# Kernel optimization log

Hardware: AMD Instinct MI355X
Metric: run time of the kernel (lower is better)

## Reference

```python
import jax, jax.numpy as jnp
import numpy as np

HID = 64
PRE = 14


def _lstm_last(x, Wih, Whh, b):
    # x: (B, T, F) batch_first; single-layer torch LSTM; returns last hidden (B, H)
    H = Whh.shape[1]
    def step(carry, xt):
        h, c = carry
        g = xt @ Wih.T + h @ Whh.T + b  # gates order i,f,g,o (torch convention)
        i, f, gg, o = jnp.split(g, 4, axis=-1)
        c = jax.nn.sigmoid(f) * c + jax.nn.sigmoid(i) * jnp.tanh(gg)
        h = jax.nn.sigmoid(o) * jnp.tanh(c)
        return (h, c), None
    h0 = jnp.zeros((x.shape[0], H), x.dtype)
    (h, _), _ = jax.lax.scan(step, (h0, h0), jnp.swapaxes(x, 0, 1))
    return h


def _sircell(beta, gamma, c, sir):
    # beta,gamma: (B,N,1); c: (B,N,N); sir: (B,N,3); beta_incorporated=False branch
    eps = 1e-8
    S, I, R = sir[..., 0:1], sir[..., 1:2], sir[..., 2:3]
    Ntot = jnp.maximum(S + I + R, eps)
    infection = c @ I                      # (B,N,1) graph diffusion of infected
    dS = -beta * S / Ntot * infection
    dI = -dS - gamma * I
    dR = gamma * I
    S_t = jnp.maximum(S + dS, 0.0)
    I_t = jnp.maximum(I + dI, 0.0)
    R_t = jnp.maximum(R + dR, 0.0)
    scale = Ntot / jnp.maximum(S_t + I_t + R_t, eps)
    I_new = jnp.maximum(-dS, 0.0)
    return jnp.concatenate([I_new, S_t * scale, I_t * scale, R_t * scale], axis=-1)


def reference(x_s, x, bWih, bWhh, bb, bfW, bfb, gWih, gWhh, gb, gfW, gfb, cWih, cWhh, cb, cfW, cfb):
    B, T, N, F = x_s.shape
    P = bfW.shape[0]
    xs = jnp.transpose(x_s, (0, 2, 1, 3)).reshape(B * N, T, F)
    betas = jax.nn.sigmoid(_lstm_last(xs, bWih, bWhh, bb) @ bfW.T + bfb).reshape(B, N, P, 1)
    gammas = jax.nn.sigmoid(_lstm_last(xs, gWih, gWhh, gb) @ gfW.T + gfb).reshape(B, N, P, 1)
    xst = jnp.transpose(x_s, (0, 2, 1, 3))                       # (B,N,T,F)
    Hi = jnp.broadcast_to(xst[:, :, None], (B, N, N, T, F))
    Hj = jnp.broadcast_to(xst[:, None], (B, N, N, T, F))
    edge = jnp.concatenate([Hi, Hj], -1).reshape(B * N * N, T, 2 * F)
    cij = jax.nn.sigmoid(_lstm_last(edge, cWih, cWhh, cb) @ cfW.T + cfb).reshape(B, N, N, P)
    cij = jax.nn.softmax(jnp.transpose(cij, (0, 3, 1, 2)), axis=-1)  # (B,P,N,N)
    cs = jnp.transpose(cij, (0, 2, 1, 3))                            # (B,N,P,N)

    def step(sir, inp):
        bt, gt, ct = inp
        nsir = _sircell(bt, gt, ct, sir)
        return nsir[:, :, 1:], nsir

    _, outs = jax.lax.scan(
        step, x[:, -1],
        (jnp.transpose(betas, (2, 0, 1, 3)),
         jnp.transpose(gammas, (2, 0, 1, 3)),
         jnp.transpose(cs, (2, 0, 1, 3))))
    out = jnp.transpose(outs, (1, 0, 2, 3))                          # (B,P,N,4)
    epi = jnp.transpose(jnp.concatenate([betas, gammas, cs], -1), (0, 2, 1, 3))  # (B,P,N,N+2)
    return out[..., 2:3], epi, out[..., 1:], out[..., 0:1]


def setup_inputs() -> dict:
    key = jax.random.key(0)
    ks = jax.random.split(key, 20)
    B, T, N, F = 4, 12, 128, 3
    H, P = HID, PRE
    s = 1.0 / np.sqrt(H)
    def u(k, shape):
        return jax.random.uniform(k, shape, jnp.float32, -s, s)
    inp = {
        'x_s': jax.random.normal(ks[0], (B, T, N, F), jnp.float32),
        'x': jax.random.uniform(ks[1], (B, T, N, F), jnp.float32),
        'bWih': u(ks[2], (4 * H, F)), 'bWhh': u(ks[3], (4 * H, H)), 'bb': u(ks[4], (4 * H,)),
        'bfW': u(ks[5], (P, H)), 'bfb': u(ks[6], (P,)),
        'gWih': u(ks[7], (4 * H, F)), 'gWhh': u(ks[8], (4 * H, H)), 'gb': u(ks[9], (4 * H,)),
        'gfW': u(ks[10], (P, H)), 'gfb': u(ks[11], (P,)),
        'cWih': u(ks[12], (4 * H, 2 * F)), 'cWhh': u(ks[13], (4 * H, H)), 'cb': u(ks[14], (4 * H,)),
        'cfW': u(ks[15], (P, H)), 'cfb': u(ks[16], (P,)),
    }
    return inp
```

## Files before the change

kernel.cpp:

```cpp
#include <hip/hip_runtime.h>

#define TT 12
#define NN 128
#define BB 4
#define PP 14

typedef __attribute__((ext_vector_type(8))) short short8;
typedef __attribute__((ext_vector_type(4))) float f32x4;
typedef __attribute__((ext_vector_type(2))) float float2v;
typedef __attribute__((ext_vector_type(2))) unsigned uint2v;

__device__ inline unsigned short f2bf(float x){
  unsigned u = __builtin_bit_cast(unsigned, x);
  u += 0x7fffu + ((u >> 16) & 1u);
  return (unsigned short)(u >> 16);
}
__device__ inline float bf2f(unsigned short h){
  unsigned u = ((unsigned)h) << 16;
  return __builtin_bit_cast(float, u);
}
__device__ inline float fexp2(float x){ return __builtin_amdgcn_exp2f(x); }
__device__ inline float sigf(float x){ return __builtin_amdgcn_rcpf(1.0f + fexp2(x * -1.44269504f)); }

__device__ inline float2v exp2v(float2v x){
  float2v r; r[0]=__builtin_amdgcn_exp2f(x[0]); r[1]=__builtin_amdgcn_exp2f(x[1]); return r;
}
__device__ inline float2v rcpv(float2v x){
  float2v r; r[0]=__builtin_amdgcn_rcpf(x[0]); r[1]=__builtin_amdgcn_rcpf(x[1]); return r;
}
__device__ inline float2v sigp(float2v xp){ return rcpv(1.0f + exp2v(xp)); }
__device__ inline float2v tanhp(float2v xp){ return 1.0f - 2.0f*rcpv(1.0f + exp2v(xp)); }

__global__ __launch_bounds__(256) void lstm_all(
    const float* __restrict__ x_s,
    const float* __restrict__ bWih, const float* __restrict__ bWhh, const float* __restrict__ bb_,
    const float* __restrict__ bfW,  const float* __restrict__ bfb,
    const float* __restrict__ gWih, const float* __restrict__ gWhh, const float* __restrict__ gb_,
    const float* __restrict__ gfW,  const float* __restrict__ gfb,
    const float* __restrict__ cWih, const float* __restrict__ cWhh, const float* __restrict__ cb_,
    const float* __restrict__ cfW,  const float* __restrict__ cfb,
    float* __restrict__ out_epi,
    float* __restrict__ betas_ws, float* __restrict__ gammas_ws)
{
  __shared__ __align__(16) char hbuf[2*4096];
  __shared__ __align__(16) unsigned short xext[TT*32*8];
  __shared__ float fw_lds[PP*64];
  __shared__ float fb_lds[PP];

  const int tid = threadIdx.x;
  const int l = tid & 63, w = tid >> 6;
  const int col = l & 15, q = l >> 4;

  const int rot = (col & 7) << 4;
  const int r0offA = col*128 + ((  0 + (q<<4) + rot) & 127);
  const int r1offA = col*128 + (( 64 + (q<<4) + rot) & 127);
  const int wroffA = col*128 + ((w*32 + q*8 + rot) & 127);
  const int r0offB = r0offA + 2048;
  const int r1offB = r1offA + 2048;
  const int wroffB = wroffA + 2048;

  int g0 = blockIdx.x << 1;
  int mode; const float *Wih, *Whh, *bias, *fW, *fb;
  if (g0 < 4096)      { mode=0; Wih=cWih; Whh=cWhh; bias=cb_; fW=cfW; fb=cfb; }
  else if (g0 < 4128) { mode=1; g0-=4096; Wih=bWih; Whh=bWhh; bias=bb_; fW=bfW; fb=bfb; }
  else                { mode=2; g0-=4128; Wih=gWih; Whh=gWhh; bias=gb_; fW=gfW; fb=gfb; }

  int b, i=0, s0;
  if (mode==0) { b = g0 >> 10; int rem = g0 & 1023; i = rem >> 3; s0 = (rem & 7) << 4; }
  else         { b = g0 >> 3; s0 = (g0 & 7) << 4; }

  for (int task = tid; task < TT*32; task += 256) {
    int t = task >> 5, m = task & 31;
    unsigned short* dst = &xext[(t*32+m)*8];
    float v0=0,v1=0,v2=0,v3=0,v4=0,v5=0,v6=0,v7=0;
    if (mode==0) {
      const float* xi = x_s + ((b*TT + t)*NN + i)*3;
      const float* xj = x_s + ((b*TT + t)*NN + (s0+m))*3;
      v0=xi[0]; v1=xi[1]; v2=xi[2]; v3=xj[0]; v4=xj[1]; v5=xj[2]; v6=1.f;
    } else {
      const float* xn = x_s + ((b*TT + t)*NN + (s0+m))*3;
      v0=xn[0]; v1=xn[1]; v2=xn[2]; v3=1.f;
    }
    dst[0]=f2bf(v0); dst[1]=f2bf(v1); dst[2]=f2bf(v2); dst[3]=f2bf(v3);
    dst[4]=f2bf(v4); dst[5]=f2bf(v5); dst[6]=f2bf(v6); dst[7]=f2bf(v7);
  }
  for (int idx = tid; idx < 1024; idx += 256) ((unsigned*)hbuf)[idx] = 0;
  for (int idx = tid; idx < PP*64; idx += 256) fw_lds[idx] = fW[idx];
  if (tid < PP) fb_lds[tid] = fb[tid];

  short8 Aw[4][2]; short8 Ax[4];
  #pragma unroll
  for (int gt = 0; gt < 4; ++gt) {
    float sc = (gt==2) ? 2.88539008f : -1.44269504f;
    int gate = gt*64 + w*16 + col;
    #pragma unroll
    for (int kt = 0; kt < 2; ++kt) {
      const float* src = Whh + gate*64 + kt*32 + q*8;
      short8 fr;
      #pragma unroll
      for (int jj = 0; jj < 8; ++jj) fr[jj] = (short)f2bf(src[jj]*sc);
      Aw[gt][kt] = fr;
    }
    short8 ax = {0,0,0,0,0,0,0,0};
    if (q == 0) {
      if (mode==0) {
        ax[0]=(short)f2bf(Wih[gate*6+0]*sc); ax[1]=(short)f2bf(Wih[gate*6+1]*sc); ax[2]=(short)f2bf(Wih[gate*6+2]*sc);
        ax[3]=(short)f2bf(Wih[gate*6+3]*sc); ax[4]=(short)f2bf(Wih[gate*6+4]*sc); ax[5]=(short)f2bf(Wih[gate*6+5]*sc);
        ax[6]=(short)f2bf(bias[gate]*sc);
      } else {
        ax[0]=(short)f2bf(Wih[gate*3+0]*sc); ax[1]=(short)f2bf(Wih[gate*3+1]*sc); ax[2]=(short)f2bf(Wih[gate*3+2]*sc);
        ax[3]=(short)f2bf(bias[gate]*sc);
      }
    }
    Ax[gt] = ax;
  }

  __syncthreads();

  float2v cA0 = {0.f,0.f}, cA1 = {0.f,0.f}, cB0 = {0.f,0.f}, cB1 = {0.f,0.f};
  const short8 zero8 = {0,0,0,0,0,0,0,0};

#define MM(acc, aop, bop) acc = __builtin_amdgcn_mfma_f32_16x16x32_bf16(aop, bop, acc, 0,0,0)

  for (int t = 0; t < TT; ++t) {
    const char* rb = hbuf + ((t & 1) ? 4096 : 0);
    char* wbp      = hbuf + ((t & 1) ? 0 : 4096);
    short8 b0a = *(const short8*)(rb + r0offA);
    short8 b1a = *(const short8*)(rb + r1offA);
    short8 b0b = *(const short8*)(rb + r0offB);
    short8 b1b = *(const short8*)(rb + r1offB);
    short8 bxa = zero8, bxb = zero8;
    if (l < 16) {
      bxa = *(const short8*)&xext[(t*32 + col)*8];
      bxb = *(const short8*)&xext[(t*32 + 16 + col)*8];
    }
    f32x4 Fa = {0.f,0.f,0.f,0.f}, Ia = Fa, Ga = Fa, Oa = Fa;
    f32x4 Fb = Fa, Ib = Fa, Gb = Fa, Ob = Fa;
    MM(Fa, Aw[1][0], b0a); MM(Fb, Aw[1][0], b0b);
    MM(Ia, Aw[0][0], b0a); MM(Ib, Aw[0][0], b0b);
    MM(Ga, Aw[2][0], b0a); MM(Gb, Aw[2][0], b0b);
    MM(Oa, Aw[3][0], b0a); MM(Ob, Aw[3][0], b0b);
    MM(Fa, Aw[1][1], b1a); MM(Fb, Aw[1][1], b1b);
    MM(Ia, Aw[0][1], b1a); MM(Ib, Aw[0][1], b1b);
    MM(Ga, Aw[2][1], b1a); MM(Gb, Aw[2][1], b1b);
    MM(Oa, Aw[3][1], b1a); MM(Ob, Aw[3][1], b1b);
    MM(Fa, Ax[1], bxa);    MM(Fb, Ax[1], bxb);
    MM(Ia, Ax[0], bxa);    MM(Ib, Ax[0], bxb);
    MM(Ga, Ax[2], bxa);    MM(Gb, Ax[2], bxb);
    MM(Oa, Ax[3], bxa);    MM(Ob, Ax[3], bxb);

    {
      float2v f0 = {Fa[0],Fa[1]}, f1 = {Fa[2],Fa[3]};
      float2v i0 = {Ia[0],Ia[1]}, i1 = {Ia[2],Ia[3]};
      float2v g0v = {Ga[0],Ga[1]}, g1v = {Ga[2],Ga[3]};
      float2v o0 = {Oa[0],Oa[1]}, o1 = {Oa[2],Oa[3]};
      cA0 = sigp(f0)*cA0 + sigp(i0)*tanhp(g0v);
      cA1 = sigp(f1)*cA1 + sigp(i1)*tanhp(g1v);
      float2v tc0 = 1.0f - 2.0f*rcpv(1.0f + exp2v(cA0 * 2.88539008f));
      float2v tc1 = 1.0f - 2.0f*rcpv(1.0f + exp2v(cA1 * 2.88539008f));
      float2v h0 = sigp(o0)*tc0;
      float2v h1 = sigp(o1)*tc1;
      unsigned plo, phi;
      asm("v_cvt_pk_bf16_f32 %0, %1, %2" : "=v"(plo) : "v"(h0[0]), "v"(h0[1]));
      asm("v_cvt_pk_bf16_f32 %0, %1, %2" : "=v"(phi) : "v"(h1[0]), "v"(h1[1]));
      uint2v pv = {plo, phi};
      *(uint2v*)(wbp + wroffA) = pv;
    }
    {
      float2v f0 = {Fb[0],Fb[1]}, f1 = {Fb[2],Fb[3]};
      float2v i0 = {Ib[0],Ib[1]}, i1 = {Ib[2],Ib[3]};
      float2v g0v = {Gb[0],Gb[1]}, g1v = {Gb[2],Gb[3]};
      float2v o0 = {Ob[0],Ob[1]}, o1 = {Ob[2],Ob[3]};
      cB0 = sigp(f0)*cB0 + sigp(i0)*tanhp(g0v);
      cB1 = sigp(f1)*cB1 + sigp(i1)*tanhp(g1v);
      float2v tc0 = 1.0f - 2.0f*rcpv(1.0f + exp2v(cB0 * 2.88539008f));
      float2v tc1 = 1.0f - 2.0f*rcpv(1.0f + exp2v(cB1 * 2.88539008f));
      float2v h0 = sigp(o0)*tc0;
      float2v h1 = sigp(o1)*tc1;
      unsigned plo, phi;
      asm("v_cvt_pk_bf16_f32 %0, %1, %2" : "=v"(plo) : "v"(h0[0]), "v"(h0[1]));
      asm("v_cvt_pk_bf16_f32 %0, %1, %2" : "=v"(phi) : "v"(h1[0]), "v"(h1[1]));
      uint2v pv = {plo, phi};
      *(uint2v*)(wbp + wroffB) = pv;
    }
    __syncthreads();
  }
#undef MM

  const char* hfin = hbuf;
  for (int task = tid; task < 32*PP; task += 256) {
    int seq = task & 31, p = task >> 5;
    int rot2 = (seq & 7) << 4;
    float dot = fb_lds[p];
    #pragma unroll
    for (int kc = 0; kc < 8; ++kc) {
      short8 v = *(const short8*)(hfin + seq*128 + (((kc<<4) + rot2) & 127));
      #pragma unroll
      for (int jj = 0; jj < 8; ++jj)
        dot += bf2f((unsigned short)v[jj]) * fw_lds[p*64 + kc*8 + jj];
    }
    float val = sigf(dot);
    if (mode==0) {
      out_epi[(size_t)((b*PP + p)*NN + i)*130 + 2 + (s0+seq)] = val;
    } else if (mode==1) {
      betas_ws[(b*NN + s0+seq)*PP + p] = val;
    } else {
      gammas_ws[(b*NN + s0+seq)*PP + p] = val;
    }
  }
}

__global__ __launch_bounds__(256) void softmax_epi(
    const float* __restrict__ betas_ws, const float* __restrict__ gammas_ws,
    float* __restrict__ out_epi)
{
  int row = blockIdx.x*4 + (threadIdx.x >> 6);
  int l = threadIdx.x & 63;
  int b = row / (PP*NN); int rem = row - b*(PP*NN); int p = rem >> 7; int i = rem & 127;
  float* epi = out_epi + (size_t)row*130;
  float v0 = epi[2+l], v1 = epi[2+64+l];
  float m = fmaxf(v0, v1);
  #pragma unroll
  for (int off = 32; off; off >>= 1) m = fmaxf(m, __shfl_xor(m, off));
  float e0 = fexp2((v0-m)*1.44269504f), e1 = fexp2((v1-m)*1.44269504f);
  float s = e0 + e1;
  #pragma unroll
  for (int off = 32; off; off >>= 1) s += __shfl_xor(s, off);
  float inv = 1.0f / s;
  epi[2+l] = e0*inv; epi[2+64+l] = e1*inv;
  if (l == 0) epi[0] = betas_ws[(b*NN+i)*PP + p];
  if (l == 1) epi[1] = gammas_ws[(b*NN+i)*PP + p];
}

__global__ __launch_bounds__(1024) void sir_scan(
    const float* __restrict__ x,
    const float* __restrict__ betas_ws, const float* __restrict__ gammas_ws,
    const float* __restrict__ epi,
    float* __restrict__ out0, float* __restrict__ out2, float* __restrict__ out3)
{
  __shared__ float Ish[NN];
  int b = blockIdx.x;
  int tid = threadIdx.x;
  int i = tid >> 3, q = tid & 7;
  const float* x0 = x + ((b*TT + 11)*NN + i)*3;
  float S = x0[0], I = x0[1], R = x0[2];
  if (q == 0) Ish[i] = I;

  float2v v[8], vn[8];
  {
    const float* crow = epi + (size_t)((b*PP + 0)*NN + i)*130 + 2 + q*16;
    #pragma unroll
    for (int jj = 0; jj < 8; ++jj) v[jj] = *(const float2v*)(crow + jj*2);
  }
  __syncthreads();
  for (int p = 0; p < PP; ++p) {
    if (p+1 < PP) {
      const float* crow = epi + (size_t)((b*PP + p+1)*NN + i)*130 + 2 + q*16;
      #pragma unroll
      for (int jj = 0; jj < 8; ++jj) vn[jj] = *(const float2v*)(crow + jj*2);
    }
    float part = 0.f;
    #pragma unroll
    for (int jj = 0; jj < 8; ++jj)
      part += v[jj][0]*Ish[q*16 + jj*2] + v[jj][1]*Ish[q*16 + jj*2 + 1];
    part += __shfl_xor(part, 1);
    part += __shfl_xor(part, 2);
    part += __shfl_xor(part, 4);
    __syncthreads();
    if (q == 0) {
      float beta  = betas_ws[(b*NN+i)*PP + p];
      float gamma = gammas_ws[(b*NN+i)*PP + p];
      float Ntot = fmaxf(S+I+R, 1e-8f);
      float dS = -beta*S/Ntot*part;
      float dI = -dS - gamma*I;
      float dR = gamma*I;
      float St = fmaxf(S+dS, 0.f), It = fmaxf(I+dI, 0.f), Rt = fmaxf(R+dR, 0.f);
      float scale = Ntot / fmaxf(St+It+Rt, 1e-8f);
      float Inew = fmaxf(-dS, 0.f);
      int o = (b*PP+p)*NN + i;
      float Sn = St*scale, In = It*scale, Rn = Rt*scale;
      out0[o] = In;
      out2[o*3+0] = Sn; out2[o*3+1] = In; out2[o*3+2] = Rn;
      out3[o] = Inew;
      S = Sn; I = In; R = Rn;
      Ish[i] = I;
    }
    #pragma unroll
    for (int jj = 0; jj < 8; ++jj) v[jj] = vn[jj];
    __syncthreads();
  }
}

extern "C" void kernel_launch(void* const* d_in, const int* in_sizes, int n_in,
                              void* d_out, int out_size, void* d_ws, size_t ws_size,
                              hipStream_t stream) {
  const float* x_s  = (const float*)d_in[0];
  const float* x    = (const float*)d_in[1];
  const float* bWih = (const float*)d_in[2];
  const float* bWhh = (const float*)d_in[3];
  const float* bb_  = (const float*)d_in[4];
  const float* bfW  = (const float*)d_in[5];
  const float* bfb  = (const float*)d_in[6];
  const float* gWih = (const float*)d_in[7];
  const float* gWhh = (const float*)d_in[8];
  const float* gb_  = (const float*)d_in[9];
  const float* gfW  = (const float*)d_in[10];
  const float* gfb  = (const float*)d_in[11];
  const float* cWih = (const float*)d_in[12];
  const float* cWhh = (const float*)d_in[13];
  const float* cb_  = (const float*)d_in[14];
  const float* cfW  = (const float*)d_in[15];
  const float* cfb  = (const float*)d_in[16];

  float* out  = (float*)d_out;
  float* out0 = out;
  float* epi  = out + 7168;
  float* out2 = out + 7168 + 931840;
  float* out3 = out + 7168 + 931840 + 21504;
  float* betas_ws  = (float*)d_ws;
  float* gammas_ws = betas_ws + 7168;

  hipLaunchKernelGGL(lstm_all, dim3(2080), dim3(256), 0, stream,
      x_s, bWih,bWhh,bb_,bfW,bfb, gWih,gWhh,gb_,gfW,gfb, cWih,cWhh,cb_,cfW,cfb,
      epi, betas_ws, gammas_ws);
  hipLaunchKernelGGL(softmax_epi, dim3(1792), dim3(256), 0, stream,
      betas_ws, gammas_ws, epi);
  hipLaunchKernelGGL(sir_scan, dim3(4), dim3(1024), 0, stream,
      x, betas_ws, gammas_ws, epi, out0, out2, out3);
}
```

Before: 113.3 us.

## Fuse softmax into SIR scan, merge LSTM cell transcendentals, drop lane guard

```diff
diff --git a/kernel.cpp b/kernel.cpp
--- a/kernel.cpp
+++ b/kernel.cpp
@@ -20,7 +20,8 @@
   return __builtin_bit_cast(float, u);
 }
 __device__ inline float fexp2(float x){ return __builtin_amdgcn_exp2f(x); }
-__device__ inline float sigf(float x){ return __builtin_amdgcn_rcpf(1.0f + fexp2(x * -1.44269504f)); }
+__device__ inline float frcp(float x){ return __builtin_amdgcn_rcpf(x); }
+__device__ inline float sigf(float x){ return frcp(1.0f + fexp2(x * -1.44269504f)); }
 
 __device__ inline float2v exp2v(float2v x){
   float2v r; r[0]=__builtin_amdgcn_exp2f(x[0]); r[1]=__builtin_amdgcn_exp2f(x[1]); return r;
@@ -28,8 +29,6 @@
 __device__ inline float2v rcpv(float2v x){
   float2v r; r[0]=__builtin_amdgcn_rcpf(x[0]); r[1]=__builtin_amdgcn_rcpf(x[1]); return r;
 }
-__device__ inline float2v sigp(float2v xp){ return rcpv(1.0f + exp2v(xp)); }
-__device__ inline float2v tanhp(float2v xp){ return 1.0f - 2.0f*rcpv(1.0f + exp2v(xp)); }
 
 __global__ __launch_bounds__(256) void lstm_all(
     const float* __restrict__ x_s,
@@ -118,9 +117,16 @@
   __syncthreads();
 
   float2v cA0 = {0.f,0.f}, cA1 = {0.f,0.f}, cB0 = {0.f,0.f}, cB1 = {0.f,0.f};
-  const short8 zero8 = {0,0,0,0,0,0,0,0};
 
 #define MM(acc, aop, bop) acc = __builtin_amdgcn_mfma_f32_16x16x32_bf16(aop, bop, acc, 0,0,0)
+#define CELL(cvar, hvar, fF, fI, fG, fO) { \
+    float2v Ei = exp2v(fI), Ef = exp2v(fF), Eg = exp2v(fG), Eo = exp2v(fO); \
+    float2v t1 = (Ei + 1.0f) * (Eg + 1.0f); \
+    float2v pf = Ef + 1.0f; \
+    float2v num = cvar * t1 + pf * (Eg - 1.0f); \
+    cvar = num * rcpv(pf * t1); \
+    float2v Ec = exp2v(cvar * 2.88539008f); \
+    hvar = (Ec - 1.0f) * rcpv((Ec + 1.0f) * (Eo + 1.0f)); }
 
   for (int t = 0; t < TT; ++t) {
     const char* rb = hbuf + ((t & 1) ? 4096 : 0);
@@ -129,11 +135,8 @@
     short8 b1a = *(const short8*)(rb + r1offA);
     short8 b0b = *(const short8*)(rb + r0offB);
     short8 b1b = *(const short8*)(rb + r1offB);
-    short8 bxa = zero8, bxb = zero8;
-    if (l < 16) {
-      bxa = *(const short8*)&xext[(t*32 + col)*8];
-      bxb = *(const short8*)&xext[(t*32 + 16 + col)*8];
-    }
+    short8 bxa = *(const short8*)&xext[(t*32 + col)*8];
+    short8 bxb = *(const short8*)&xext[(t*32 + 16 + col)*8];
     f32x4 Fa = {0.f,0.f,0.f,0.f}, Ia = Fa, Ga = Fa, Oa = Fa;
     f32x4 Fb = Fa, Ib = Fa, Gb = Fa, Ob = Fa;
     MM(Fa, Aw[1][0], b0a); MM(Fb, Aw[1][0], b0b);
@@ -154,12 +157,9 @@
       float2v i0 = {Ia[0],Ia[1]}, i1 = {Ia[2],Ia[3]};
       float2v g0v = {Ga[0],Ga[1]}, g1v = {Ga[2],Ga[3]};
       float2v o0 = {Oa[0],Oa[1]}, o1 = {Oa[2],Oa[3]};
-      cA0 = sigp(f0)*cA0 + sigp(i0)*tanhp(g0v);
-      cA1 = sigp(f1)*cA1 + sigp(i1)*tanhp(g1v);
-      float2v tc0 = 1.0f - 2.0f*rcpv(1.0f + exp2v(cA0 * 2.88539008f));
-      float2v tc1 = 1.0f - 2.0f*rcpv(1.0f + exp2v(cA1 * 2.88539008f));
-      float2v h0 = sigp(o0)*tc0;
-      float2v h1 = sigp(o1)*tc1;
+      float2v h0, h1;
+      CELL(cA0, h0, f0, i0, g0v, o0);
+      CELL(cA1, h1, f1, i1, g1v, o1);
       unsigned plo, phi;
       asm("v_cvt_pk_bf16_f32 %0, %1, %2" : "=v"(plo) : "v"(h0[0]), "v"(h0[1]));
       asm("v_cvt_pk_bf16_f32 %0, %1, %2" : "=v"(phi) : "v"(h1[0]), "v"(h1[1]));
@@ -171,12 +171,9 @@
       float2v i0 = {Ib[0],Ib[1]}, i1 = {Ib[2],Ib[3]};
       float2v g0v = {Gb[0],Gb[1]}, g1v = {Gb[2],Gb[3]};
       float2v o0 = {Ob[0],Ob[1]}, o1 = {Ob[2],Ob[3]};
-      cB0 = sigp(f0)*cB0 + sigp(i0)*tanhp(g0v);
-      cB1 = sigp(f1)*cB1 + sigp(i1)*tanhp(g1v);
-      float2v tc0 = 1.0f - 2.0f*rcpv(1.0f + exp2v(cB0 * 2.88539008f));
-      float2v tc1 = 1.0f - 2.0f*rcpv(1.0f + exp2v(cB1 * 2.88539008f));
-      float2v h0 = sigp(o0)*tc0;
-      float2v h1 = sigp(o1)*tc1;
+      float2v h0, h1;
+      CELL(cB0, h0, f0, i0, g0v, o0);
+      CELL(cB1, h1, f1, i1, g1v, o1);
       unsigned plo, phi;
       asm("v_cvt_pk_bf16_f32 %0, %1, %2" : "=v"(plo) : "v"(h0[0]), "v"(h0[1]));
       asm("v_cvt_pk_bf16_f32 %0, %1, %2" : "=v"(phi) : "v"(h1[0]), "v"(h1[1]));
@@ -186,6 +183,7 @@
     __syncthreads();
   }
 #undef MM
+#undef CELL
 
   const char* hfin = hbuf;
   for (int task = tid; task < 32*PP; task += 256) {
@@ -204,38 +202,18 @@
       out_epi[(size_t)((b*PP + p)*NN + i)*130 + 2 + (s0+seq)] = val;
     } else if (mode==1) {
       betas_ws[(b*NN + s0+seq)*PP + p] = val;
+      out_epi[(size_t)((b*PP + p)*NN + (s0+seq))*130 + 0] = val;
     } else {
       gammas_ws[(b*NN + s0+seq)*PP + p] = val;
-    }
-  }
-}
-
-__global__ __launch_bounds__(256) void softmax_epi(
-    const float* __restrict__ betas_ws, const float* __restrict__ gammas_ws,
-    float* __restrict__ out_epi)
-{
-  int row = blockIdx.x*4 + (threadIdx.x >> 6);
-  int l = threadIdx.x & 63;
-  int b = row / (PP*NN); int rem = row - b*(PP*NN); int p = rem >> 7; int i = rem & 127;
-  float* epi = out_epi + (size_t)row*130;
-  float v0 = epi[2+l], v1 = epi[2+64+l];
-  float m = fmaxf(v0, v1);
-  #pragma unroll
-  for (int off = 32; off; off >>= 1) m = fmaxf(m, __shfl_xor(m, off));
-  float e0 = fexp2((v0-m)*1.44269504f), e1 = fexp2((v1-m)*1.44269504f);
-  float s = e0 + e1;
-  #pragma unroll
-  for (int off = 32; off; off >>= 1) s += __shfl_xor(s, off);
-  float inv = 1.0f / s;
-  epi[2+l] = e0*inv; epi[2+64+l] = e1*inv;
-  if (l == 0) epi[0] = betas_ws[(b*NN+i)*PP + p];
-  if (l == 1) epi[1] = gammas_ws[(b*NN+i)*PP + p];
+      out_epi[(size_t)((b*PP + p)*NN + (s0+seq))*130 + 1] = val;
+    }
+  }
 }
 
 __global__ __launch_bounds__(1024) void sir_scan(
     const float* __restrict__ x,
     const float* __restrict__ betas_ws, const float* __restrict__ gammas_ws,
-    const float* __restrict__ epi,
+    float* __restrict__ epi,
     float* __restrict__ out0, float* __restrict__ out2, float* __restrict__ out3)
 {
   __shared__ float Ish[NN];
@@ -259,13 +237,33 @@
       #pragma unroll
       for (int jj = 0; jj < 8; ++jj) vn[jj] = *(const float2v*)(crow + jj*2);
     }
+    float2v e[8];
+    float s = 0.f;
+    #pragma unroll
+    for (int jj = 0; jj < 8; ++jj) {
+      float2v ev; ev[0] = fexp2(v[jj][0]*1.44269504f); ev[1] = fexp2(v[jj][1]*1.44269504f);
+      e[jj] = ev; s += ev[0] + ev[1];
+    }
+    s += __shfl_xor(s, 1);
+    s += __shfl_xor(s, 2);
+    s += __shfl_xor(s, 4);
+    float inv = frcp(s);
     float part = 0.f;
     #pragma unroll
     for (int jj = 0; jj < 8; ++jj)
-      part += v[jj][0]*Ish[q*16 + jj*2] + v[jj][1]*Ish[q*16 + jj*2 + 1];
+      part += e[jj][0]*Ish[q*16 + jj*2] + e[jj][1]*Ish[q*16 + jj*2 + 1];
     part += __shfl_xor(part, 1);
     part += __shfl_xor(part, 2);
     part += __shfl_xor(part, 4);
+    part *= inv;
+    {
+      float* crow = epi + (size_t)((b*PP + p)*NN + i)*130 + 2 + q*16;
+      #pragma unroll
+      for (int jj = 0; jj < 8; ++jj) {
+        float2v nv = {e[jj][0]*inv, e[jj][1]*inv};
+        *(float2v*)(crow + jj*2) = nv;
+      }
+    }
     __syncthreads();
     if (q == 0) {
       float beta  = betas_ws[(b*NN+i)*PP + p];
@@ -323,8 +321,6 @@
   hipLaunchKernelGGL(lstm_all, dim3(2080), dim3(256), 0, stream,
       x_s, bWih,bWhh,bb_,bfW,bfb, gWih,gWhh,gb_,gfW,gfb, cWih,cWhh,cb_,cfW,cfb,
       epi, betas_ws, gammas_ws);
-  hipLaunchKernelGGL(softmax_epi, dim3(1792), dim3(256), 0, stream,
-      betas_ws, gammas_ws, epi);
   hipLaunchKernelGGL(sir_scan, dim3(4), dim3(1024), 0, stream,
       x, betas_ws, gammas_ws, epi, out0, out2, out3);
 }
```

Measured after the change: 141.9 us. +25.2%, slower.
